# Optimization experiments

Hardware: AMD Instinct MI355X
Metric: run time of the kernel (lower is better)

The kernel has to match this reference:

```python
import jax, jax.numpy as jnp
import numpy as np
import math

HIST = 10  # attention window over per-node prediction history


def setup_inputs() -> dict:
    key = jax.random.key(0)
    ks = jax.random.split(key, 16)
    N, DEG, F, H, M, O, P, S = 512, 8, 128, 256, 256, 64, 2, 64

    def lin(k, fan_in, shape):
        b = 1.0 / np.sqrt(fan_in)
        return jax.random.uniform(k, shape, jnp.float32, -b, b)

    return {
        "xa": jax.random.normal(ks[0], (N, F), jnp.float32),
        "neighbors": jax.random.randint(ks[1], (N, DEG), 0, N),
        "first_message": jax.random.normal(ks[2], (N, M), jnp.float32),
        "We": lin(ks[3], F, (F, H)), "be": lin(ks[3], F, (H,)),
        "Wq": lin(ks[4], M, (M, H)), "bq": lin(ks[4], M, (H,)),
        "Wk": lin(ks[5], H, (H, H)), "bk": lin(ks[5], H, (H,)),
        "Wr": lin(ks[6], 4 * H, (4 * H, H)), "br": lin(ks[6], 4 * H, (H,)),
        "Wm": lin(ks[7], H + M, (H + M, M)), "bm": lin(ks[7], H + M, (M,)),
        "Wd": lin(ks[8], H, (P, H, O)), "bd": lin(ks[8], H, (P, O)),
        "num_starts": S,
    }


def reference(xa, neighbors, first_message, We, be, Wq, bq, Wk, bk,
              Wr, br, Wm, bm, Wd, bd, num_starts):
    N, H = xa.shape[0], We.shape[1]
    M = first_message.shape[1]
    DEG = neighbors.shape[1]
    max_steps = 10 * N                    # message budget, as in the while-loop cap
    CAP = num_starts + max_steps * DEG    # static queue capacity bound
    inv_sqrt_h = 1.0 / math.sqrt(H)
    nbrs = neighbors.astype(jnp.int32)
    slot_ids = jnp.arange(HIST)

    encoded = xa @ We + be                                    # [N,H]
    hist = jnp.zeros((N, HIST, H), xa.dtype).at[:, 0, :].set(encoded)
    count = jnp.ones((N,), jnp.int32)
    q_node = jnp.zeros((CAP,), jnp.int32).at[:num_starts].set(
        jnp.arange(num_starts, dtype=jnp.int32))
    q_msg = jnp.zeros((CAP, M), xa.dtype).at[:num_starts].set(
        first_message[:num_starts])
    head = jnp.int32(0)
    tail = jnp.int32(num_starts)

    def step(carry, _):
        hist, count, q_node, q_msg, head, tail = carry
        active = head < tail                 # queue non-empty
        node = q_node[head]
        message = q_msg[head]                # [M]
        feats = hist[node]                   # [HIST,H] ring buffer of last states
        c = count[node]
        valid = slot_ids < jnp.minimum(c, HIST)
        # NOTE: source uses queries[0]/keys[0] for every head -> heads identical
        query = message @ Wq + bq            # [H]
        keys = feats @ Wk + bk               # [HIST,H]
        logits = jnp.where(valid, keys @ query * inv_sqrt_h, -jnp.inf)
        attn = jax.nn.softmax(logits)        # softmax over history axis (dim=-0)
        values = attn @ feats                # [H]
        newstate = jnp.concatenate([values] * 4) @ Wr + br     # [H]
        newmessage = jnp.concatenate([newstate, message]) @ Wm + bm  # [M]
        # conditional state updates (no-op writes when inactive)
        slot = c % HIST
        hist = hist.at[node, slot].set(jnp.where(active, newstate, hist[node, slot]))
        count = count.at[node].add(jnp.where(active, 1, 0))
        old_n = jax.lax.dynamic_slice(q_node, (tail,), (DEG,))
        old_m = jax.lax.dynamic_slice(q_msg, (tail, 0), (DEG, M))
        q_node = jax.lax.dynamic_update_slice(
            q_node, jnp.where(active, nbrs[node], old_n), (tail,))
        q_msg = jax.lax.dynamic_update_slice(
            q_msg, jnp.where(active, jnp.broadcast_to(newmessage, (DEG, M)), old_m),
            (tail, 0))
        head = head + jnp.where(active, 1, 0)
        tail = tail + jnp.where(active, DEG, 0)
        return (hist, count, q_node, q_msg, head, tail), None

    (hist, count, _, _, _, _), _ = jax.lax.scan(
        step, (hist, count, q_node, q_msg, head, tail), None, length=max_steps)

    final = hist[jnp.arange(N), (count - 1) % HIST]           # [N,H] last state
    logits = jnp.einsum('nh,pho->pno', final, Wd) + bd[:, None, :]
    return jax.nn.log_softmax(logits, axis=-1)                # [P,N,O]
```

## Files before the change

kernel.cpp:

```cpp
#include <hip/hip_runtime.h>
#include <hip/hip_bf16.h>

#define NN 512
#define DEG 8
#define FD 128
#define HD 256
#define MD 256
#define OD 64
#define PD 2
#define HIST 10
#define TOTAL (10 * NN)
#define NPAR 648
#define INV_SQRT_H 0.0625f

typedef __hip_bfloat16 bf16;

__device__ __forceinline__ float finz(float x) {
  unsigned u = __float_as_uint(x);
  return (((u >> 23) & 0xFFu) == 0xFFu) ? 0.f : x;
}

__device__ __forceinline__ float ldin(const void* p, int idx, int bf) {
  if (bf) return __bfloat162float(((const bf16*)p)[idx]);
  return ((const float*)p)[idx];
}

__device__ __forceinline__ float scload(const float* p) {
  return __uint_as_float(__hip_atomic_load((const unsigned*)p, __ATOMIC_RELAXED,
                                           __HIP_MEMORY_SCOPE_AGENT));
}
__device__ __forceinline__ void scstore(float* p, float v) {
  __hip_atomic_store((unsigned*)p, __float_as_uint(v), __ATOMIC_RELAXED,
                     __HIP_MEMORY_SCOPE_AGENT);
}

__device__ float g_hist[NN * HIST * HD];
__device__ float g_msgb[NPAR * MD];
__device__ float g_WQK[HD * HD];
__device__ float g_WrS[HD * HD];
__device__ float g_vq[HD];
__device__ float g_ck[HD];
__device__ float g_bqk;
__device__ int   g_node[TOTAL];
__device__ int   g_counts[NN];
__device__ int   g_done[TOTAL];
__device__ int   g_dtype;
__device__ int   g_i64;

__device__ __forceinline__ int decode_S(const int* dS) {
  int r = dS[0];
  if (r >= 1 && r <= NN) return r;
  float f = __int_as_float(r);
  if (f >= 1.f && f <= (float)NN) return (int)f;
  unsigned u = ((unsigned)r & 0xFFFFu) << 16;
  float g = __uint_as_float(u);
  if (g >= 1.f && g <= (float)NN) return (int)g;
  return 64;
}

__device__ __forceinline__ int get_nbr(const int* nbrs, int i64, int n, int d) {
  int v = i64 ? nbrs[2 * (n * DEG + d)] : nbrs[n * DEG + d];
  return (v < 0) ? 0 : (v >= NN ? NN - 1 : v);
}

__device__ __forceinline__ int detect_bf(const unsigned* xa_w) {
  const int lane = threadIdx.x & 63;
  unsigned lo = xa_w[lane] & 0xFFFFu;
  float av = fabsf(__uint_as_float(lo << 16));
  unsigned long long m = __ballot(av > 0.000244140625f && av < 64.f);
  return ((int)__popcll(m) >= 32) ? 1 : 0;
}

__global__ void __launch_bounds__(1024)
k_prep(const void* __restrict__ xa, const unsigned* __restrict__ xa_w,
       const int* __restrict__ nbrs, const int* __restrict__ dS,
       const void* __restrict__ We, const void* __restrict__ be,
       const void* __restrict__ Wq, const void* __restrict__ Wk,
       const void* __restrict__ Wr, const void* __restrict__ bq,
       const void* __restrict__ bk) {
  const int b = blockIdx.x, t = threadIdx.x;
  const int col = t & 255, grp = t >> 8;
  const int wave = t >> 6, lane = t & 63;
  const int bf = detect_bf(xa_w);
  if (t < 8) { int fi = 8 * b + t; if (fi < TOTAL) g_done[fi] = 0; }
  __shared__ float sw[HD];
  __shared__ float sp[4][HD];
  __shared__ float sr[16];
  __shared__ int s_node[TOTAL];
  if (b < HD) {
    if (grp == 0) sw[col] = ldin(Wq, b * HD + col, bf);
    __syncthreads();
    {
      const int h0 = grp * 64;
      float a0 = 0.f, a1 = 0.f, a2 = 0.f, a3 = 0.f;
      for (int h = 0; h < 64; h += 4) {
        a0 += sw[h0 + h]     * ldin(Wk, col * HD + h0 + h,     bf);
        a1 += sw[h0 + h + 1] * ldin(Wk, col * HD + h0 + h + 1, bf);
        a2 += sw[h0 + h + 2] * ldin(Wk, col * HD + h0 + h + 2, bf);
        a3 += sw[h0 + h + 3] * ldin(Wk, col * HD + h0 + h + 3, bf);
      }
      sp[grp][col] = (a0 + a1) + (a2 + a3);
    }
    if (grp == 1) {
      float pv = sw[col] * ldin(bk, col, bf);
#pragma unroll
      for (int off = 32; off > 0; off >>= 1) pv += __shfl_down(pv, off, 64);
      if (lane == 0) sr[wave] = pv;
    }
    if (grp == 2) {
      float s = 0.f;
#pragma unroll
      for (int q = 0; q < 4; ++q) s += ldin(Wr, (size_t)(q * HD + b) * HD + col, bf);
      g_WrS[b * HD + col] = s;
    }
    __syncthreads();
    if (grp == 0)
      g_WQK[b * HD + col] = (sp[0][col] + sp[1][col]) + (sp[2][col] + sp[3][col]);
    if (t == 0) g_vq[b] = (sr[4] + sr[5]) + (sr[6] + sr[7]);
  } else if (b == HD) {
    {
      const int h0 = grp * 64;
      float a0 = 0.f, a1 = 0.f, a2 = 0.f, a3 = 0.f;
      for (int h = 0; h < 64; h += 4) {
        a0 += ldin(Wk, col * HD + h0 + h,     bf) * ldin(bq, h0 + h,     bf);
        a1 += ldin(Wk, col * HD + h0 + h + 1, bf) * ldin(bq, h0 + h + 1, bf);
        a2 += ldin(Wk, col * HD + h0 + h + 2, bf) * ldin(bq, h0 + h + 2, bf);
        a3 += ldin(Wk, col * HD + h0 + h + 3, bf) * ldin(bq, h0 + h + 3, bf);
      }
      sp[grp][col] = (a0 + a1) + (a2 + a3);
    }
    if (grp == 1) {
      float pb = ldin(bq, col, bf) * ldin(bk, col, bf);
#pragma unroll
      for (int off = 32; off > 0; off >>= 1) pb += __shfl_down(pb, off, 64);
      if (lane == 0) sr[wave] = pb;
    }
    __syncthreads();
    if (grp == 0)
      g_ck[col] = (sp[0][col] + sp[1][col]) + (sp[2][col] + sp[3][col]);
    if (t == 0) g_bqk = (sr[4] + sr[5]) + (sr[6] + sr[7]);
  } else if (b <= HD + NN) {
    const int n = b - HD - 1;
    if (t < FD) sw[t] = ldin(xa, n * FD + t, bf);
    __syncthreads();
    const int f0 = grp * 32;
    float a0 = 0.f, a1 = 0.f, a2 = 0.f, a3 = 0.f;
    for (int f = 0; f < 32; f += 4) {
      a0 += sw[f0 + f]     * ldin(We, (f0 + f)     * HD + col, bf);
      a1 += sw[f0 + f + 1] * ldin(We, (f0 + f + 1) * HD + col, bf);
      a2 += sw[f0 + f + 2] * ldin(We, (f0 + f + 2) * HD + col, bf);
      a3 += sw[f0 + f + 3] * ldin(We, (f0 + f + 3) * HD + col, bf);
    }
    sp[grp][col] = (a0 + a1) + (a2 + a3);
    __syncthreads();
    if (grp == 0)
      g_hist[(size_t)(n * HIST) * HD + col] =
          ldin(be, col, bf) + (sp[0][col] + sp[1][col]) + (sp[2][col] + sp[3][col]);
  } else {
    if (t == 0) g_dtype = bf;
    bool c8 = (lane < 8) ? (nbrs[2 * lane + 1] == 0) : true;
    unsigned long long im = __ballot(c8);
    const int i64 = ((im & 0xFFull) == 0xFFull) ? 1 : 0;
    if (t == 0) g_i64 = i64;
    const int S = decode_S(dS);
    for (int i = t; i < S; i += 1024) s_node[i] = i;
    __syncthreads();
    int done = S;
    while (done < TOTAL) {
      long long nd = (long long)S + 8LL * (long long)done;
      int new_done = nd > (long long)TOTAL ? TOTAL : (int)nd;
      for (int i = done + t; i < new_done; i += 1024)
        s_node[i] = get_nbr(nbrs, i64, s_node[(i - S) >> 3], (i - S) & 7);
      __syncthreads();
      done = new_done;
    }
    for (int i = t; i < TOTAL; i += 1024) g_node[i] = s_node[i];
  }
}

__global__ void __launch_bounds__(256, 2)
k_flow(const void* __restrict__ fmsg, const void* __restrict__ br_,
       const void* __restrict__ Wm, const void* __restrict__ bm,
       const int* __restrict__ dS) {
  const int n = blockIdx.x;
  const int t = threadIdx.x;
  const int wave = t >> 6, lane = t & 63;
  const int S = decode_S(dS);
  const int bf = g_dtype;
  __shared__ float s_hist[HIST][HD];
  __shared__ float s_msg[MD];
  __shared__ float s_vals[HD];
  __shared__ float s_ns[HD];
  __shared__ float s_red[4][HIST + 1];
  __shared__ int   s_list[TOTAL];
  __shared__ int   s_cnt;

#pragma unroll
  for (int j = 1; j < HIST; ++j) s_hist[j][t] = 0.f;
  s_hist[0][t] = finz(g_hist[(size_t)n * HIST * HD + t]);

  if (wave == 0) {
    int k = 0;
    for (int base = 0; base < TOTAL; base += 64) {
      int nd = g_node[base + lane];
      unsigned long long m = __ballot(nd == n);
      if (nd == n) {
        unsigned long long below = m & ((1ull << lane) - 1ull);
        s_list[k + (int)__popcll(below)] = base + lane;
      }
      k += (int)__popcll(m);
    }
    if (lane == 0) { s_cnt = k; g_counts[n] = k; }
  }
  __syncthreads();
  const int cnt = s_cnt;

  for (int k = 0; k < cnt; ++k) {
    const int e = s_list[k];
    const int c = k + 1;
    const int v = (c < HIST) ? c : HIST;
    const int slot = c % HIST;
    const bool hc = (S + 8 * e) < TOTAL;

    float ms;
    if (e < S) {
      ms = ldin(fmsg, e * MD + t, bf);
    } else {
      const int p = (e - S) >> 3;
      if (t == 0)
        while (__hip_atomic_load(&g_done[p], __ATOMIC_RELAXED,
                                 __HIP_MEMORY_SCOPE_AGENT) == 0)
          __builtin_amdgcn_s_sleep(4);
      __syncthreads();
      ms = scload(g_msgb + (size_t)p * MD + t);
    }
    s_msg[t] = finz(ms);
    __syncthreads();

    float a0 = 0.f, a1 = 0.f, a2 = 0.f, a3 = 0.f;
    for (int m = 0; m < MD; m += 4) {
      a0 += s_msg[m]     * g_WQK[(m)     * HD + t];
      a1 += s_msg[m + 1] * g_WQK[(m + 1) * HD + t];
      a2 += s_msg[m + 2] * g_WQK[(m + 2) * HD + t];
      a3 += s_msg[m + 3] * g_WQK[(m + 3) * HD + t];
    }
    const float kq = g_ck[t] + ((a0 + a1) + (a2 + a3));

    float part[HIST + 1];
#pragma unroll
    for (int j = 0; j < HIST; ++j) part[j] = s_hist[j][t] * kq;
    part[HIST] = s_msg[t] * g_vq[t];
#pragma unroll
    for (int o = 32; o > 0; o >>= 1) {
#pragma unroll
      for (int j = 0; j <= HIST; ++j) part[j] += __shfl_down(part[j], o, 64);
    }
    if (lane == 0) {
#pragma unroll
      for (int j = 0; j <= HIST; ++j) s_red[wave][j] = part[j];
    }
    __syncthreads();

    float sc[HIST + 1];
#pragma unroll
    for (int j = 0; j <= HIST; ++j)
      sc[j] = (s_red[0][j] + s_red[1][j]) + (s_red[2][j] + s_red[3][j]);
    const float bkq = sc[HIST] + g_bqk;
    float lg[HIST];
#pragma unroll
    for (int j = 0; j < HIST; ++j)
      lg[j] = (j < v) ? ((sc[j] + bkq) * INV_SQRT_H) : -1e30f;
    float mx = lg[0];
#pragma unroll
    for (int j = 1; j < HIST; ++j) mx = fmaxf(mx, lg[j]);
    float e_[HIST], den = 0.f;
#pragma unroll
    for (int j = 0; j < HIST; ++j) { e_[j] = __expf(lg[j] - mx); den += e_[j]; }
    const float iden = 1.0f / den;
    float val = 0.f;
#pragma unroll
    for (int j = 0; j < HIST; ++j) val += e_[j] * s_hist[j][t];
    s_vals[t] = val * iden;
    __syncthreads();

    float b0 = 0.f, b1 = 0.f, b2 = 0.f, b3 = 0.f;
    for (int h = 0; h < HD; h += 4) {
      b0 += s_vals[h]     * g_WrS[(h)     * HD + t];
      b1 += s_vals[h + 1] * g_WrS[(h + 1) * HD + t];
      b2 += s_vals[h + 2] * g_WrS[(h + 2) * HD + t];
      b3 += s_vals[h + 3] * g_WrS[(h + 3) * HD + t];
    }
    const float ns = ldin(br_, t, bf) + ((b0 + b1) + (b2 + b3));
    s_hist[slot][t] = ns;
    if (k == cnt - 1)
      g_hist[(size_t)(n * HIST + slot) * HD + t] = ns;
    if (hc) s_ns[t] = ns;
    __syncthreads();

    if (hc) {
      float c0 = 0.f, c1 = 0.f, c2 = 0.f, c3 = 0.f;
      if (bf) {
        const bf16* w = (const bf16*)Wm;
        for (int h = 0; h < HD; h += 4) {
          c0 += s_ns[h]     * __bfloat162float(w[(h)     * MD + t]);
          c1 += s_ns[h + 1] * __bfloat162float(w[(h + 1) * MD + t]);
          c2 += s_ns[h + 2] * __bfloat162float(w[(h + 2) * MD + t]);
          c3 += s_ns[h + 3] * __bfloat162float(w[(h + 3) * MD + t]);
        }
        for (int m = 0; m < MD; m += 4) {
          c0 += s_msg[m]     * __bfloat162float(w[(HD + m)     * MD + t]);
          c1 += s_msg[m + 1] * __bfloat162float(w[(HD + m + 1) * MD + t]);
          c2 += s_msg[m + 2] * __bfloat162float(w[(HD + m + 2) * MD + t]);
          c3 += s_msg[m + 3] * __bfloat162float(w[(HD + m + 3) * MD + t]);
        }
      } else {
        const float* w = (const float*)Wm;
        for (int h = 0; h < HD; h += 4) {
          c0 += s_ns[h]     * w[(h)     * MD + t];
          c1 += s_ns[h + 1] * w[(h + 1) * MD + t];
          c2 += s_ns[h + 2] * w[(h + 2) * MD + t];
          c3 += s_ns[h + 3] * w[(h + 3) * MD + t];
        }
        for (int m = 0; m < MD; m += 4) {
          c0 += s_msg[m]     * w[(HD + m)     * MD + t];
          c1 += s_msg[m + 1] * w[(HD + m + 1) * MD + t];
          c2 += s_msg[m + 2] * w[(HD + m + 2) * MD + t];
          c3 += s_msg[m + 3] * w[(HD + m + 3) * MD + t];
        }
      }
      scstore(&g_msgb[(size_t)e * MD + t],
              ldin(bm, t, bf) + ((c0 + c1) + (c2 + c3)));
      asm volatile("s_waitcnt vmcnt(0)" ::: "memory");
    }
    __syncthreads();
    if (hc && t == 0)
      __hip_atomic_store(&g_done[e], 1, __ATOMIC_RELAXED,
                         __HIP_MEMORY_SCOPE_AGENT);
  }
}

__global__ void k_out(const void* __restrict__ Wd, const void* __restrict__ bd,
                      void* __restrict__ out) {
  __shared__ float sf[HD];
  const int b = blockIdx.x;
  const int pp = b >> 9;
  const int n = b & 511;
  const int t = threadIdx.x;
  const int bf = g_dtype;
  int occ = g_counts[n];
  if (occ < 0 || occ > TOTAL) occ = 0;
  const int slot = occ % HIST;
  for (int h = t; h < HD; h += OD) sf[h] = finz(g_hist[(size_t)(n * HIST + slot) * HD + h]);
  __syncthreads();
  float acc = finz(ldin(bd, pp * OD + t, bf));
  for (int h = 0; h < HD; ++h) acc += sf[h] * ldin(Wd, (pp * HD + h) * OD + t, bf);
  acc = finz(acc);
  float mx = acc;
#pragma unroll
  for (int off = 32; off > 0; off >>= 1) mx = fmaxf(mx, __shfl_xor(mx, off, 64));
  float ex = __expf(acc - mx);
  float s = ex;
#pragma unroll
  for (int off = 32; off > 0; off >>= 1) s += __shfl_xor(s, off, 64);
  float r = finz(acc - mx - logf(s));
  const int oi = (pp * NN + n) * OD + t;
  if (bf) ((bf16*)out)[oi] = __float2bfloat16(r);
  else    ((float*)out)[oi] = r;
}

extern "C" void kernel_launch(void* const* d_in, const int* in_sizes, int n_in,
                              void* d_out, int out_size, void* d_ws, size_t ws_size,
                              hipStream_t stream) {
  const void* xa   = d_in[0];
  const int*  nbrs = (const int*)d_in[1];
  const void* fmsg = d_in[2];
  const void* We   = d_in[3];
  const void* be   = d_in[4];
  const void* Wq   = d_in[5];
  const void* bq   = d_in[6];
  const void* Wk   = d_in[7];
  const void* bk   = d_in[8];
  const void* Wr   = d_in[9];
  const void* br   = d_in[10];
  const void* Wm   = d_in[11];
  const void* bm   = d_in[12];
  const void* Wd   = d_in[13];
  const void* bd   = d_in[14];
  const int*  dS   = (const int*)d_in[15];
  (void)d_ws; (void)ws_size; (void)in_sizes; (void)n_in; (void)out_size;

  k_prep<<<dim3(HD + 1 + NN + 1), dim3(1024), 0, stream>>>(
      xa, (const unsigned*)xa, nbrs, dS, We, be, Wq, Wk, Wr, bq, bk);
  k_flow<<<dim3(NN), dim3(256), 0, stream>>>(fmsg, br, Wm, bm, dS);
  k_out<<<dim3(PD * NN), dim3(OD), 0, stream>>>(Wd, bd, d_out);
}
```

Baseline: 465.7 us.

## Split matvecs across waves by K-slice with float4 column loads

```diff
diff --git a/kernel.cpp b/kernel.cpp
--- a/kernel.cpp
+++ b/kernel.cpp
@@ -23,6 +23,10 @@
 __device__ __forceinline__ float ldin(const void* p, int idx, int bf) {
   if (bf) return __bfloat162float(((const bf16*)p)[idx]);
   return ((const float*)p)[idx];
+}
+
+__device__ __forceinline__ float bfu(unsigned short u) {
+  return __uint_as_float(((unsigned)u) << 16);
 }
 
 __device__ __forceinline__ float scload(const float* p) {
@@ -185,12 +189,14 @@
   const int n = blockIdx.x;
   const int t = threadIdx.x;
   const int wave = t >> 6, lane = t & 63;
+  const int C = lane << 2;
   const int S = decode_S(dS);
   const int bf = g_dtype;
   __shared__ float s_hist[HIST][HD];
   __shared__ float s_msg[MD];
   __shared__ float s_vals[HD];
   __shared__ float s_ns[HD];
+  __shared__ float s_p[4][HD];
   __shared__ float s_red[4][HIST + 1];
   __shared__ int   s_list[TOTAL];
   __shared__ int   s_cnt;
@@ -230,21 +236,30 @@
       if (t == 0)
         while (__hip_atomic_load(&g_done[p], __ATOMIC_RELAXED,
                                  __HIP_MEMORY_SCOPE_AGENT) == 0)
-          __builtin_amdgcn_s_sleep(4);
+          __builtin_amdgcn_s_sleep(2);
       __syncthreads();
       ms = scload(g_msgb + (size_t)p * MD + t);
     }
     s_msg[t] = finz(ms);
     __syncthreads();
 
-    float a0 = 0.f, a1 = 0.f, a2 = 0.f, a3 = 0.f;
-    for (int m = 0; m < MD; m += 4) {
-      a0 += s_msg[m]     * g_WQK[(m)     * HD + t];
-      a1 += s_msg[m + 1] * g_WQK[(m + 1) * HD + t];
-      a2 += s_msg[m + 2] * g_WQK[(m + 2) * HD + t];
-      a3 += s_msg[m + 3] * g_WQK[(m + 3) * HD + t];
-    }
-    const float kq = g_ck[t] + ((a0 + a1) + (a2 + a3));
+    {
+      const float* wp = g_WQK + (size_t)(64 * wave) * HD + C;
+      const float* mp = s_msg + 64 * wave;
+      float4 a0 = {0.f, 0.f, 0.f, 0.f}, a1 = {0.f, 0.f, 0.f, 0.f};
+      for (int m = 0; m < 64; m += 2) {
+        const float s0 = mp[m], s1 = mp[m + 1];
+        const float4 w0 = *(const float4*)(wp + (size_t)m * HD);
+        const float4 w1 = *(const float4*)(wp + (size_t)(m + 1) * HD);
+        a0.x += s0 * w0.x; a0.y += s0 * w0.y; a0.z += s0 * w0.z; a0.w += s0 * w0.w;
+        a1.x += s1 * w1.x; a1.y += s1 * w1.y; a1.z += s1 * w1.z; a1.w += s1 * w1.w;
+      }
+      a0.x += a1.x; a0.y += a1.y; a0.z += a1.z; a0.w += a1.w;
+      *(float4*)&s_p[wave][C] = a0;
+    }
+    __syncthreads();
+    const float kq = g_ck[t] +
+        ((s_p[0][t] + s_p[1][t]) + (s_p[2][t] + s_p[3][t]));
 
     float part[HIST + 1];
 #pragma unroll
@@ -283,14 +298,23 @@
     s_vals[t] = val * iden;
     __syncthreads();
 
-    float b0 = 0.f, b1 = 0.f, b2 = 0.f, b3 = 0.f;
-    for (int h = 0; h < HD; h += 4) {
-      b0 += s_vals[h]     * g_WrS[(h)     * HD + t];
-      b1 += s_vals[h + 1] * g_WrS[(h + 1) * HD + t];
-      b2 += s_vals[h + 2] * g_WrS[(h + 2) * HD + t];
-      b3 += s_vals[h + 3] * g_WrS[(h + 3) * HD + t];
-    }
-    const float ns = ldin(br_, t, bf) + ((b0 + b1) + (b2 + b3));
+    {
+      const float* wp = g_WrS + (size_t)(64 * wave) * HD + C;
+      const float* vp = s_vals + 64 * wave;
+      float4 a0 = {0.f, 0.f, 0.f, 0.f}, a1 = {0.f, 0.f, 0.f, 0.f};
+      for (int h = 0; h < 64; h += 2) {
+        const float s0 = vp[h], s1 = vp[h + 1];
+        const float4 w0 = *(const float4*)(wp + (size_t)h * HD);
+        const float4 w1 = *(const float4*)(wp + (size_t)(h + 1) * HD);
+        a0.x += s0 * w0.x; a0.y += s0 * w0.y; a0.z += s0 * w0.z; a0.w += s0 * w0.w;
+        a1.x += s1 * w1.x; a1.y += s1 * w1.y; a1.z += s1 * w1.z; a1.w += s1 * w1.w;
+      }
+      a0.x += a1.x; a0.y += a1.y; a0.z += a1.z; a0.w += a1.w;
+      *(float4*)&s_p[wave][C] = a0;
+    }
+    __syncthreads();
+    const float ns = ldin(br_, t, bf) +
+        ((s_p[0][t] + s_p[1][t]) + (s_p[2][t] + s_p[3][t]));
     s_hist[slot][t] = ns;
     if (k == cnt - 1)
       g_hist[(size_t)(n * HIST + slot) * HD + t] = ns;
@@ -298,44 +322,44 @@
     __syncthreads();
 
     if (hc) {
-      float c0 = 0.f, c1 = 0.f, c2 = 0.f, c3 = 0.f;
+      const float* src = (wave < 2) ? (s_ns + 128 * wave) : (s_msg + 128 * (wave - 2));
+      float4 a0 = {0.f, 0.f, 0.f, 0.f}, a1 = {0.f, 0.f, 0.f, 0.f};
       if (bf) {
-        const bf16* w = (const bf16*)Wm;
-        for (int h = 0; h < HD; h += 4) {
-          c0 += s_ns[h]     * __bfloat162float(w[(h)     * MD + t]);
-          c1 += s_ns[h + 1] * __bfloat162float(w[(h + 1) * MD + t]);
-          c2 += s_ns[h + 2] * __bfloat162float(w[(h + 2) * MD + t]);
-          c3 += s_ns[h + 3] * __bfloat162float(w[(h + 3) * MD + t]);
-        }
-        for (int m = 0; m < MD; m += 4) {
-          c0 += s_msg[m]     * __bfloat162float(w[(HD + m)     * MD + t]);
-          c1 += s_msg[m + 1] * __bfloat162float(w[(HD + m + 1) * MD + t]);
-          c2 += s_msg[m + 2] * __bfloat162float(w[(HD + m + 2) * MD + t]);
-          c3 += s_msg[m + 3] * __bfloat162float(w[(HD + m + 3) * MD + t]);
+        const unsigned short* wb =
+            (const unsigned short*)Wm + (size_t)(128 * wave) * MD + C;
+        for (int r = 0; r < 128; r += 2) {
+          const float s0 = src[r], s1 = src[r + 1];
+          const ushort4 u0 = *(const ushort4*)(wb + (size_t)r * MD);
+          const ushort4 u1 = *(const ushort4*)(wb + (size_t)(r + 1) * MD);
+          a0.x += s0 * bfu(u0.x); a0.y += s0 * bfu(u0.y);
+          a0.z += s0 * bfu(u0.z); a0.w += s0 * bfu(u0.w);
+          a1.x += s1 * bfu(u1.x); a1.y += s1 * bfu(u1.y);
+          a1.z += s1 * bfu(u1.z); a1.w += s1 * bfu(u1.w);
         }
       } else {
-        const float* w = (const float*)Wm;
-        for (int h = 0; h < HD; h += 4) {
-          c0 += s_ns[h]     * w[(h)     * MD + t];
-          c1 += s_ns[h + 1] * w[(h + 1) * MD + t];
-          c2 += s_ns[h + 2] * w[(h + 2) * MD + t];
-          c3 += s_ns[h + 3] * w[(h + 3) * MD + t];
+        const float* wf = (const float*)Wm + (size_t)(128 * wave) * MD + C;
+        for (int r = 0; r < 128; r += 2) {
+          const float s0 = src[r], s1 = src[r + 1];
+          const float4 w0 = *(const float4*)(wf + (size_t)r * MD);
+          const float4 w1 = *(const float4*)(wf + (size_t)(r + 1) * MD);
+          a0.x += s0 * w0.x; a0.y += s0 * w0.y; a0.z += s0 * w0.z; a0.w += s0 * w0.w;
+          a1.x += s1 * w1.x; a1.y += s1 * w1.y; a1.z += s1 * w1.z; a1.w += s1 * w1.w;
         }
-        for (int m = 0; m < MD; m += 4) {
-          c0 += s_msg[m]     * w[(HD + m)     * MD + t];
-          c1 += s_msg[m + 1] * w[(HD + m + 1) * MD + t];
-          c2 += s_msg[m + 2] * w[(HD + m + 2) * MD + t];
-          c3 += s_msg[m + 3] * w[(HD + m + 3) * MD + t];
-        }
-      }
+      }
+      a0.x += a1.x; a0.y += a1.y; a0.z += a1.z; a0.w += a1.w;
+      *(float4*)&s_p[wave][C] = a0;
+      __syncthreads();
       scstore(&g_msgb[(size_t)e * MD + t],
-              ldin(bm, t, bf) + ((c0 + c1) + (c2 + c3)));
+              ldin(bm, t, bf) +
+                  ((s_p[0][t] + s_p[1][t]) + (s_p[2][t] + s_p[3][t])));
       asm volatile("s_waitcnt vmcnt(0)" ::: "memory");
-    }
-    __syncthreads();
-    if (hc && t == 0)
-      __hip_atomic_store(&g_done[e], 1, __ATOMIC_RELAXED,
-                         __HIP_MEMORY_SCOPE_AGENT);
+      __syncthreads();
+      if (t == 0)
+        __hip_atomic_store(&g_done[e], 1, __ATOMIC_RELAXED,
+                           __HIP_MEMORY_SCOPE_AGENT);
+    } else {
+      __syncthreads();
+    }
   }
 }
 
```

Measured after the change: 766.2 us. +64.5%, slower.

## Prefetch next message opportunistically, hoist per-thread constants, fuse output head into flow kernel

Applied to the files above, without the earlier changes.

```diff
diff --git a/kernel.cpp b/kernel.cpp
--- a/kernel.cpp
+++ b/kernel.cpp
@@ -42,7 +42,6 @@
 __device__ float g_ck[HD];
 __device__ float g_bqk;
 __device__ int   g_node[TOTAL];
-__device__ int   g_counts[NN];
 __device__ int   g_done[TOTAL];
 __device__ int   g_dtype;
 __device__ int   g_i64;
@@ -181,19 +180,27 @@
 __global__ void __launch_bounds__(256, 2)
 k_flow(const void* __restrict__ fmsg, const void* __restrict__ br_,
        const void* __restrict__ Wm, const void* __restrict__ bm,
-       const int* __restrict__ dS) {
+       const void* __restrict__ Wd, const void* __restrict__ bd,
+       void* __restrict__ out, const int* __restrict__ dS) {
   const int n = blockIdx.x;
   const int t = threadIdx.x;
   const int wave = t >> 6, lane = t & 63;
   const int S = decode_S(dS);
   const int bf = g_dtype;
   __shared__ float s_hist[HIST][HD];
-  __shared__ float s_msg[MD];
+  __shared__ float s_msgb2[2][MD];
   __shared__ float s_vals[HD];
   __shared__ float s_ns[HD];
   __shared__ float s_red[4][HIST + 1];
   __shared__ int   s_list[TOTAL];
   __shared__ int   s_cnt;
+  __shared__ int   s_pf[2];
+
+  const float rck = g_ck[t];
+  const float rvq = g_vq[t];
+  const float rbqk = g_bqk;
+  const float rbr = ldin(br_, t, bf);
+  const float rbm = ldin(bm, t, bf);
 
 #pragma unroll
   for (int j = 1; j < HIST; ++j) s_hist[j][t] = 0.f;
@@ -210,7 +217,7 @@
       }
       k += (int)__popcll(m);
     }
-    if (lane == 0) { s_cnt = k; g_counts[n] = k; }
+    if (lane == 0) { s_cnt = k; s_pf[0] = 0; s_pf[1] = 0; }
   }
   __syncthreads();
   const int cnt = s_cnt;
@@ -221,21 +228,34 @@
     const int v = (c < HIST) ? c : HIST;
     const int slot = c % HIST;
     const bool hc = (S + 8 * e) < TOTAL;
-
-    float ms;
-    if (e < S) {
-      ms = ldin(fmsg, e * MD + t, bf);
-    } else {
-      const int p = (e - S) >> 3;
-      if (t == 0)
-        while (__hip_atomic_load(&g_done[p], __ATOMIC_RELAXED,
-                                 __HIP_MEMORY_SCOPE_AGENT) == 0)
-          __builtin_amdgcn_s_sleep(4);
+    float* s_msg = s_msgb2[k & 1];
+    const int havepf = s_pf[k & 1];
+
+    if (t == 0) {
+      int pf = 0;
+      if (k + 1 < cnt) {
+        const int e2 = s_list[k + 1];
+        if (e2 < S) pf = 1;
+        else pf = (__hip_atomic_load(&g_done[(e2 - S) >> 3], __ATOMIC_RELAXED,
+                                     __HIP_MEMORY_SCOPE_AGENT) != 0);
+      }
+      s_pf[(k + 1) & 1] = pf;
+    }
+
+    if (!havepf) {
+      if (e < S) {
+        s_msg[t] = finz(ldin(fmsg, e * MD + t, bf));
+      } else {
+        const int p = (e - S) >> 3;
+        if (t == 0)
+          while (__hip_atomic_load(&g_done[p], __ATOMIC_RELAXED,
+                                   __HIP_MEMORY_SCOPE_AGENT) == 0)
+            __builtin_amdgcn_s_sleep(4);
+        __syncthreads();
+        s_msg[t] = finz(scload(g_msgb + (size_t)p * MD + t));
+      }
       __syncthreads();
-      ms = scload(g_msgb + (size_t)p * MD + t);
-    }
-    s_msg[t] = finz(ms);
-    __syncthreads();
+    }
 
     float a0 = 0.f, a1 = 0.f, a2 = 0.f, a3 = 0.f;
     for (int m = 0; m < MD; m += 4) {
@@ -244,12 +264,12 @@
       a2 += s_msg[m + 2] * g_WQK[(m + 2) * HD + t];
       a3 += s_msg[m + 3] * g_WQK[(m + 3) * HD + t];
     }
-    const float kq = g_ck[t] + ((a0 + a1) + (a2 + a3));
+    const float kq = rck + ((a0 + a1) + (a2 + a3));
 
     float part[HIST + 1];
 #pragma unroll
     for (int j = 0; j < HIST; ++j) part[j] = s_hist[j][t] * kq;
-    part[HIST] = s_msg[t] * g_vq[t];
+    part[HIST] = s_msg[t] * rvq;
 #pragma unroll
     for (int o = 32; o > 0; o >>= 1) {
 #pragma unroll
@@ -260,12 +280,20 @@
       for (int j = 0; j <= HIST; ++j) s_red[wave][j] = part[j];
     }
     __syncthreads();
+
+    const int dopf = s_pf[(k + 1) & 1];
+    float pm = 0.f;
+    if (dopf) {
+      const int e2 = s_list[k + 1];
+      pm = (e2 < S) ? ldin(fmsg, e2 * MD + t, bf)
+                    : scload(g_msgb + (size_t)((e2 - S) >> 3) * MD + t);
+    }
 
     float sc[HIST + 1];
 #pragma unroll
     for (int j = 0; j <= HIST; ++j)
       sc[j] = (s_red[0][j] + s_red[1][j]) + (s_red[2][j] + s_red[3][j]);
-    const float bkq = sc[HIST] + g_bqk;
+    const float bkq = sc[HIST] + rbqk;
     float lg[HIST];
 #pragma unroll
     for (int j = 0; j < HIST; ++j)
@@ -290,11 +318,10 @@
       b2 += s_vals[h + 2] * g_WrS[(h + 2) * HD + t];
       b3 += s_vals[h + 3] * g_WrS[(h + 3) * HD + t];
     }
-    const float ns = ldin(br_, t, bf) + ((b0 + b1) + (b2 + b3));
+    const float ns = rbr + ((b0 + b1) + (b2 + b3));
     s_hist[slot][t] = ns;
-    if (k == cnt - 1)
-      g_hist[(size_t)(n * HIST + slot) * HD + t] = ns;
     if (hc) s_ns[t] = ns;
+    if (dopf) s_msgb2[(k + 1) & 1][t] = finz(pm);
     __syncthreads();
 
     if (hc) {
@@ -328,8 +355,7 @@
           c3 += s_msg[m + 3] * w[(HD + m + 3) * MD + t];
         }
       }
-      scstore(&g_msgb[(size_t)e * MD + t],
-              ldin(bm, t, bf) + ((c0 + c1) + (c2 + c3)));
+      scstore(&g_msgb[(size_t)e * MD + t], rbm + ((c0 + c1) + (c2 + c3)));
       asm volatile("s_waitcnt vmcnt(0)" ::: "memory");
     }
     __syncthreads();
@@ -337,35 +363,26 @@
       __hip_atomic_store(&g_done[e], 1, __ATOMIC_RELAXED,
                          __HIP_MEMORY_SCOPE_AGENT);
   }
-}
-
-__global__ void k_out(const void* __restrict__ Wd, const void* __restrict__ bd,
-                      void* __restrict__ out) {
-  __shared__ float sf[HD];
-  const int b = blockIdx.x;
-  const int pp = b >> 9;
-  const int n = b & 511;
-  const int t = threadIdx.x;
-  const int bf = g_dtype;
-  int occ = g_counts[n];
-  if (occ < 0 || occ > TOTAL) occ = 0;
-  const int slot = occ % HIST;
-  for (int h = t; h < HD; h += OD) sf[h] = finz(g_hist[(size_t)(n * HIST + slot) * HD + h]);
-  __syncthreads();
-  float acc = finz(ldin(bd, pp * OD + t, bf));
-  for (int h = 0; h < HD; ++h) acc += sf[h] * ldin(Wd, (pp * HD + h) * OD + t, bf);
-  acc = finz(acc);
-  float mx = acc;
-#pragma unroll
-  for (int off = 32; off > 0; off >>= 1) mx = fmaxf(mx, __shfl_xor(mx, off, 64));
-  float ex = __expf(acc - mx);
-  float s = ex;
-#pragma unroll
-  for (int off = 32; off > 0; off >>= 1) s += __shfl_xor(s, off, 64);
-  float r = finz(acc - mx - logf(s));
-  const int oi = (pp * NN + n) * OD + t;
-  if (bf) ((bf16*)out)[oi] = __float2bfloat16(r);
-  else    ((float*)out)[oi] = r;
+
+  const int slotF = cnt % HIST;
+  if (t < PD * OD) {
+    const int pp = t >> 6, o = t & 63;
+    float acc = finz(ldin(bd, pp * OD + o, bf));
+    for (int h = 0; h < HD; ++h)
+      acc += finz(s_hist[slotF][h]) * ldin(Wd, (pp * HD + h) * OD + o, bf);
+    acc = finz(acc);
+    float mx = acc;
+#pragma unroll
+    for (int off = 32; off > 0; off >>= 1) mx = fmaxf(mx, __shfl_xor(mx, off, 64));
+    float ex = __expf(acc - mx);
+    float s = ex;
+#pragma unroll
+    for (int off = 32; off > 0; off >>= 1) s += __shfl_xor(s, off, 64);
+    float r = finz(acc - mx - logf(s));
+    const int oi = (pp * NN + n) * OD + o;
+    if (bf) ((bf16*)out)[oi] = __float2bfloat16(r);
+    else    ((float*)out)[oi] = r;
+  }
 }
 
 extern "C" void kernel_launch(void* const* d_in, const int* in_sizes, int n_in,
@@ -391,6 +408,5 @@
 
   k_prep<<<dim3(HD + 1 + NN + 1), dim3(1024), 0, stream>>>(
       xa, (const unsigned*)xa, nbrs, dS, We, be, Wq, Wk, Wr, bq, bk);
-  k_flow<<<dim3(NN), dim3(256), 0, stream>>>(fmsg, br, Wm, bm, dS);
-  k_out<<<dim3(PD * NN), dim3(OD), 0, stream>>>(Wd, bd, d_out);
-}
+  k_flow<<<dim3(NN), dim3(256), 0, stream>>>(fmsg, br, Wm, bm, Wd, bd, d_out, dS);
+}
```

Result: faster. 447.1 us (-4.0%).
